# Kernel optimization log

Hardware: AMD Instinct MI355X
Metric: run time of the kernel (lower is better)

The kernel has to match this reference:

```python
import jax, jax.numpy as jnp
import numpy as np
from jax.scipy.special import gammaln

BLOCK = 96          # NIQE block size at scale 1 (48 at scale 2)
KSIZE = 7           # gaussian MSCN window size
SIGMA = 7.0 / 6.0   # gaussian sigma
PAD = KSIZE // 2
NUM_FEAT = 18       # features per block per scale

# gamma grid for AGGD shape-parameter search (matches torch.arange(0.2, 10.001, 0.001))
AGGD_GRID = jnp.asarray(np.arange(0.2, 10.0 + 0.001, 0.001), dtype=jnp.float32)
R_GAM = jnp.exp(2.0 * gammaln(2.0 / AGGD_GRID) - (gammaln(1.0 / AGGD_GRID) + gammaln(3.0 / AGGD_GRID)))


def _gauss_kernel():
    m = (KSIZE - 1) / 2.0
    y, x = np.ogrid[-m:m + 1, -m:m + 1]
    h = np.exp(-(x * x + y * y) / (2.0 * SIGMA * SIGMA))
    h[h < np.finfo(h.dtype).eps * h.max()] = 0
    h = h / h.sum()
    return jnp.asarray(h, dtype=jnp.float32)[None, None]  # (1,1,7,7)

GAUSS = _gauss_kernel()


def imfilter(x):
    # replicate ('same') padding + valid conv, like _image_filter
    xp = jnp.pad(x, ((0, 0), (0, 0), (PAD, PAD), (PAD, PAD)), mode='edge')
    return jax.lax.conv_general_dilated(xp, GAUSS, (1, 1), 'VALID')


def estimate_aggd(blocks):
    # blocks: (N, k, k)
    mask_l = blocks < 0
    mask_r = blocks > 0
    cl = jnp.sum(mask_l, axis=(-1, -2)).astype(blocks.dtype)
    cr = jnp.sum(mask_r, axis=(-1, -2)).astype(blocks.dtype)
    left_std = jnp.sqrt(jnp.sum(jnp.where(mask_l, blocks, 0.0) ** 2, axis=(-1, -2)) / (cl + 1e-8))
    right_std = jnp.sqrt(jnp.sum(jnp.where(mask_r, blocks, 0.0) ** 2, axis=(-1, -2)) / (cr + 1e-8))
    gamma_hat = left_std / right_std
    rhat = jnp.mean(jnp.abs(blocks), axis=(-1, -2)) ** 2 / jnp.mean(blocks ** 2, axis=(-1, -2))
    rhat_norm = rhat * (gamma_hat ** 3 + 1.0) * (gamma_hat + 1.0) / (gamma_hat ** 2 + 1.0) ** 2
    pos = jnp.argmin(jnp.abs(R_GAM[None, :] - rhat_norm[:, None]), axis=-1)  # (N, 9801) search
    alpha = AGGD_GRID[pos]
    conv = jnp.sqrt(jnp.exp(gammaln(1.0 / alpha) - gammaln(3.0 / alpha)))
    return alpha, left_std * conv, right_std * conv


def mscn_features(blocks):
    # blocks: (N, k, k) -> (N, 18)
    alpha, lb, rb = estimate_aggd(blocks)
    feats = [alpha, (lb + rb) / 2.0]
    for sh in ((0, 1), (1, 0), (1, 1), (1, -1)):
        shifted = jnp.roll(blocks, sh, axis=(-2, -1))
        a, l, r = estimate_aggd(blocks * shifted)
        mean = (r - l) * jnp.exp(gammaln(2.0 / a) - gammaln(1.0 / a))
        feats.extend((a, mean, l, r))
    return jnp.stack(feats, axis=-1)


def blockify(img, bs):
    # img: (b,1,H,W) -> (b, nb, bs, bs); partial blocks discarded like _blockproc_torch
    b, _, h, w = img.shape
    nbh, nbw = h // bs, w // bs
    x = img[:, 0, :nbh * bs, :nbw * bs].reshape(b, nbh, bs, nbw, bs)
    return x.transpose(0, 1, 3, 2, 4).reshape(b, nbh * nbw, bs, bs)


def mscn_normalize(img):
    mu = imfilter(img)
    sigma = jnp.sqrt(jnp.abs(imfilter(img * img) - mu * mu))
    return (img - mu) / (sigma + 1.0)


def niqe_score(image, mu_pris, cov_pris):
    img = image
    feats = []
    for scale in (1, 2):
        norm = mscn_normalize(img)
        blocks = blockify(norm, BLOCK // scale)
        b, nb, k, _ = blocks.shape
        f = mscn_features(blocks.reshape(b * nb, k, k)).reshape(b, nb, NUM_FEAT)
        feats.append(f)
        if scale == 1:
            # 2x2 average-pool downsample for second scale
            bb, cc, hh, ww = img.shape
            img = img.reshape(bb, cc, hh // 2, 2, ww // 2, 2).mean(axis=(3, 5))
    feats = jnp.concatenate(feats, axis=-1)  # (b, nb, 36)
    nb = feats.shape[1]
    mu_dist = feats.mean(axis=1)                        # (b, 36)
    xm = feats - mu_dist[:, None, :]
    cov_dist = jnp.einsum('bnf,bng->bfg', xm, xm) / (nb - 1)
    cov = (cov_pris[None] + cov_dist) / 2.0
    diff = mu_pris[None, :] - mu_dist                   # (b, 36)
    invc = jnp.linalg.pinv(cov)
    quad = jnp.einsum('bf,bfg,bg->b', diff, invc, diff)
    return jnp.sqrt(jnp.maximum(quad, 0.0))


def setup_inputs() -> dict:
    key = jax.random.key(0)
    k1, k2, k3 = jax.random.split(key, 3)
    image = jax.random.uniform(k1, (16, 1, 1056, 1056), dtype=jnp.float32)
    mu_pris = jax.random.normal(k2, (36,), dtype=jnp.float32)
    a = jax.random.normal(k3, (36, 36), dtype=jnp.float32)
    cov_pris = a @ a.T / 36.0 + 0.5 * jnp.eye(36, dtype=jnp.float32)  # SPD pristine covariance
    return {'image': image, 'mu_pris': mu_pris, 'cov_pris': cov_pris}


def reference(image, mu_pris, cov_pris):
    return niqe_score(image, mu_pris, cov_pris)
```

## Files before the change

### kernel.cpp

```cpp
#include <hip/hip_runtime.h>
#include <math.h>

#define NGRID 9801
#define NB 11
#define NBLK (NB*NB)
#define BATCH 16
#define NFEAT 36

typedef float v2f __attribute__((ext_vector_type(2)));

__global__ void init_tables(float* __restrict__ rgam, float* __restrict__ convt,
                            float* __restrict__ meanf, float* __restrict__ w1d) {
    int i = blockIdx.x * blockDim.x + threadIdx.x;
    if (i < NGRID) {
        double a = (double)(float)(0.2 + 0.001 * (double)i);
        double g1 = lgamma(1.0 / a);
        double g2 = lgamma(2.0 / a);
        double g3 = lgamma(3.0 / a);
        rgam[i]  = (float)exp(2.0 * g2 - g1 - g3);
        convt[i] = (float)sqrt(exp(g1 - g3));
        meanf[i] = (float)exp(g2 - g1);
    }
    if (i == 0) {
        double g[7], s = 0.0;
        for (int k = 0; k < 7; ++k) { double d = (double)(k - 3); g[k] = exp(-d * d * 18.0 / 49.0); s += g[k]; }
        for (int k = 0; k < 7; ++k) w1d[k] = (float)(g[k] / s);
    }
}

__device__ __forceinline__ float bperm(int addr, float v) {
    return __int_as_float(__builtin_amdgcn_ds_bpermute(addr, __float_as_int(v)));
}
__device__ __forceinline__ float dpp_getL(float v) {
    return __int_as_float(__builtin_amdgcn_update_dpp(
        0, __float_as_int(v), 0x138 , 0xF, 0xF, true));
}
__device__ __forceinline__ float dpp_getR(float v) {
    return __int_as_float(__builtin_amdgcn_update_dpp(
        0, __float_as_int(v), 0x130 , 0xF, 0xF, true));
}

template <int K, bool WDS>
__global__ __launch_bounds__(256) void fused_mscn_stats(
        const float* __restrict__ img, float* __restrict__ dsout,
        const float* __restrict__ w1d, float* __restrict__ stats) {
    constexpr int NSLAB = K / 48;
    constexpr int NSTRIP = 4 / NSLAB;
    constexpr int SROWS = K / NSTRIP;
    constexpr int W = K * NB;
    constexpr int H = W;

    __shared__ float lastrow[NSTRIP][K];
    __shared__ float edgeL[NSTRIP][NSLAB][SROWS];
    __shared__ float edgeR[NSTRIP][NSLAB][SROWS];
    __shared__ float redf[4][15];
    __shared__ float redc[4][10];

    const int tid = threadIdx.x;
    const int lane = tid & 63;
    const int wv = tid >> 6;
    const int slab = wv % NSLAB;
    const int strip = wv / NSLAB;
    const int bIdx = blockIdx.x;
    const int b = blockIdx.y;
    const int bh = bIdx / NB, bw = bIdx % NB;
    const int x0 = bw * K + slab * 48;
    const int gx = x0 - 3 + lane;
    const int gxc = min(max(gx, 0), W - 1);
    const int r0 = bh * K + strip * SROWS;
    const bool act = (lane >= 3) && (lane <= 50);
    int am1 = 0, ap1 = 0;
    if constexpr (NSLAB == 1) {
        am1 = ((lane == 3) ? 50 : (lane - 1)) << 2;
        ap1 = ((lane == 50) ? 3 : (lane + 1)) << 2;
    }

    const char* baseB = (const char*)(img + (size_t)b * H * W);
    const float w0=w1d[0], w1=w1d[1], w2=w1d[2], w3=w1d[3], w4=w1d[4], w5=w1d[5], w6=w1d[6];

    int addrB = (min(max(r0 - 3, 0), H - 1) * W + gxc) * 4;
    int rowNext = r0 - 2;
    auto ld = [&]() -> float {
        float v = *(const float*)(baseB + addrB);
        addrB += (rowNext >= 1 && rowNext < H) ? (W * 4) : 0;
        ++rowNext;
        return v;
    };

    float pa0, pa1, pa2, pa4, pa5, pa6, vHp;
    auto issue_raw = [&](float v) {
        pa2 = dpp_getL(v);
        pa1 = dpp_getL(pa2);
        pa0 = dpp_getL(pa1);
        pa4 = dpp_getR(v);
        pa5 = dpp_getR(pa4);
        pa6 = dpp_getR(pa5);
        vHp = v;
    };
    auto sq2 = [](float v) -> v2f { v2f t; t.x = v; t.y = v * v; return t; };
    auto combine_raw = [&]() -> v2f {
        v2f r = sq2(pa0) * w0;
        r += sq2(pa1) * w1;
        r += sq2(pa2) * w2;
        r += sq2(vHp) * w3;
        r += sq2(pa4) * w4;
        r += sq2(pa5) * w5;
        r += sq2(pa6) * w6;
        return r;
    };

    v2f accp[5];
    float sab[5];
    #pragma unroll
    for (int s = 0; s < 5; ++s) { accp[s] = (v2f)0.f; sab[s] = 0.f; }
    int cl[5] = {0,0,0,0,0}, cr[5] = {0,0,0,0,0};

    auto upd = [&](int s, float v) {
        float vp = fmaxf(v, 0.f);
        v2f t; t.x = vp; t.y = v;
        accp[s] += t * t;
        sab[s] += fabsf(v);
        cl[s] += __popcll(__ballot(v < 0.f));
        cr[s] += __popcll(__ballot(v > 0.f));
    };

    v2f mq0,mq1,mq2,mq3,mq4,mq5,mq6;
    float rA, rB, rC, rD;
    float vN = ld();
    { float v=vN; vN=ld(); issue_raw(v); mq0=combine_raw(); }
    { float v=vN; vN=ld(); issue_raw(v); mq1=combine_raw(); }
    { float v=vN; vN=ld(); issue_raw(v); mq2=combine_raw(); }
    { float v=vN; vN=ld(); issue_raw(v); mq3=combine_raw(); rA=v; }
    { float v=vN; vN=ld(); issue_raw(v); mq4=combine_raw(); rB=v; }
    { float v=vN; vN=ld(); issue_raw(v); mq5=combine_raw(); rC=v; }
    { float v=vN; vN=ld(); issue_raw(v); mq6=combine_raw(); rD=v; }
    { float v=vN; vN=ld(); issue_raw(v); }
    float vN2 = ld();
    float vN3 = ld();
    float vN4 = ld();

    float normP = 0.f, normP2 = 0.f;
    float pendSL = 0.f, pendPL = 0.f, pendPR = 0.f;
    float firstN = 0.f, dsSave = 0.f;
    const bool dsw = WDS && (lane & 1) && (lane >= 3) && (lane <= 49);

    #pragma unroll 4
    for (int yy = 0; yy < SROWS; ++yy) {
        const int y = r0 + yy;
        if (yy > 0) {
            upd(0, normP);
            upd(1, normP * pendSL);
            upd(2, normP * normP2);
            upd(3, normP * pendPL);
            upd(4, normP * pendPR);
        }
        v2f ms = mq0 * w0;
        ms += mq1 * w1;
        ms += mq2 * w2;
        ms += mq3 * w3;
        ms += mq4 * w4;
        ms += mq5 * w5;
        ms += mq6 * w6;
        float mu = ms.x, s2 = ms.y;
        float sig = __builtin_amdgcn_sqrtf(fabsf(s2 - mu * mu));
        float nrm = (rA - mu) * __builtin_amdgcn_rcpf(sig + 1.0f);
        float cur = act ? nrm : 0.f;

        if (yy == 0) firstN = cur;
        if constexpr (NSLAB == 2) {
            if (lane == 3)  edgeL[strip][slab][yy] = cur;
            if (lane == 50) edgeR[strip][slab][yy] = cur;
        }
        if (yy == SROWS - 1 && act) lastrow[strip][slab * 48 + lane - 3] = cur;

        if constexpr (WDS) {
            float hs = rA + dpp_getR(rA);
            if ((y & 1) == 0) dsSave = hs;
            else if (dsw)
                dsout[((size_t)b * (H / 2) + (y >> 1)) * (W / 2) + (gx >> 1)] = 0.25f * (dsSave + hs);
        }

        if constexpr (NSLAB == 2) {
            pendSL = dpp_getL(cur);
            pendPL = dpp_getL(normP);
            pendPR = dpp_getR(normP);
        } else {
            pendSL = bperm(am1, cur);
            pendPL = bperm(am1, normP);
            pendPR = bperm(ap1, normP);
        }
        normP2 = normP; normP = cur;

        v2f mh = combine_raw();
        mq0=mq1; mq1=mq2; mq2=mq3; mq3=mq4; mq4=mq5; mq5=mq6; mq6=mh;

        rA=rB; rB=rC; rC=rD; rD=vHp;
        float vv = vN; vN=vN2; vN2=vN3; vN3=vN4; vN4=ld();
        issue_raw(vv);
    }
    upd(0, normP);
    upd(1, normP * pendSL);
    upd(2, normP * normP2);
    upd(3, normP * pendPL);
    upd(4, normP * pendPR);

    __syncthreads();

    {
        const int ps = (strip + NSTRIP - 1) % NSTRIP;
        int j  = slab * 48 + (lane - 3);
        int js = act ? j : 0;
        int jm1 = (js + K - 1) % K;
        int jp1 = (js + 1) % K;
        float pv  = act ? lastrow[ps][js]  : 0.f;
        float pvL = act ? lastrow[ps][jm1] : 0.f;
        float pvR = act ? lastrow[ps][jp1] : 0.f;
        upd(2, firstN * pv);
        upd(3, firstN * pvL);
        upd(4, firstN * pvR);
    }

    if constexpr (NSLAB == 2) {
        if (lane < SROWS) {
            int r = lane;
            if (slab == 0) {
                float c0  = edgeL[strip][0][r];
                float e95 = edgeR[strip][1][r];
                upd(1, c0 * e95);
                if (r > 0) {
                    upd(3, c0 * edgeR[strip][1][r - 1]);
                    upd(4, edgeR[strip][0][r] * edgeL[strip][1][r - 1]);
                }
            } else {
                float c48 = edgeL[strip][1][r];
                float e47 = edgeR[strip][0][r];
                upd(1, c48 * e47);
                if (r > 0) {
                    upd(3, c48 * edgeR[strip][0][r - 1]);
                    upd(4, edgeR[strip][1][r] * edgeL[strip][0][r - 1]);
                }
            }
        }
    }

    #pragma unroll
    for (int off = 32; off >= 1; off >>= 1)
        #pragma unroll
        for (int s = 0; s < 5; ++s) {
            accp[s].x += __shfl_down(accp[s].x, off);
            accp[s].y += __shfl_down(accp[s].y, off);
            sab[s]    += __shfl_down(sab[s],    off);
        }
    if (lane == 0) {
        #pragma unroll
        for (int s = 0; s < 5; ++s) {
            redf[wv][s*3+0] = accp[s].x;
            redf[wv][s*3+1] = accp[s].y;
            redf[wv][s*3+2] = sab[s];
            redc[wv][s*2+0] = (float)cl[s];
            redc[wv][s*2+1] = (float)cr[s];
        }
    }
    __syncthreads();
    if (tid < 15) {
        stats[((size_t)b * NBLK + bIdx) * 25 + tid] =
            redf[0][tid] + redf[1][tid] + redf[2][tid] + redf[3][tid];
    } else if (tid < 25) {
        int t = tid - 15;
        stats[((size_t)b * NBLK + bIdx) * 25 + tid] =
            redc[0][t] + redc[1][t] + redc[2][t] + redc[3][t];
    }
}

__global__ __launch_bounds__(256) void aggd_kernel(
        const float* __restrict__ stats1, const float* __restrict__ stats2,
        const float* __restrict__ rgam, const float* __restrict__ convt,
        const float* __restrict__ meanf, float* __restrict__ feats) {
    __shared__ float rg[NGRID];
    for (int i = threadIdx.x; i < NGRID; i += 256) rg[i] = rgam[i];
    __syncthreads();

    int gid = blockIdx.x * 256 + threadIdx.x;
    if (gid >= 2 * BATCH * NBLK * 5) return;
    int s = gid % 5; int t = gid / 5;
    int blk = t % NBLK; t /= NBLK;
    int b = t % BATCH; int scale = t / BATCH;

    const float* st = (scale ? stats2 : stats1) + ((size_t)b * NBLK + blk) * 25;
    float sr2 = st[s*3+0], ssq = st[s*3+1], sab = st[s*3+2];
    float cl = st[15 + 2*s], cr = st[15 + 2*s + 1];
    float sl2 = fmaxf(ssq - sr2, 0.f);
    float n = scale ? (48.f * 48.f) : (96.f * 96.f);

    float lstd = sqrtf(sl2 / (cl + 1e-8f));
    float rstd = sqrtf(sr2 / (cr + 1e-8f));
    float gh = lstd / rstd;
    float mab = sab / n;
    float msq = ssq / n;
    float rhat = mab * mab / msq;
    float g2 = gh * gh;
    float x = rhat * (gh * g2 + 1.f) * (gh + 1.f) / ((g2 + 1.f) * (g2 + 1.f));

    int lo = 0, hi = NGRID;
    while (lo < hi) {
        int mid = (lo + hi) >> 1;
        if (rg[mid] < x) lo = mid + 1; else hi = mid;
    }
    int gi;
    if (lo <= 0) gi = 0;
    else if (lo >= NGRID) gi = NGRID - 1;
    else {
        float dlo = x - rg[lo - 1];
        float dhi = rg[lo] - x;
        gi = (dlo <= dhi) ? lo - 1 : lo;
    }

    float alpha = (float)(0.2 + 0.001 * (double)gi);
    float cv = convt[gi];
    float lb = lstd * cv, rb = rstd * cv;
    float* fo = feats + ((size_t)b * NBLK + blk) * NFEAT + (scale ? 18 : 0);
    if (s == 0) {
        fo[0] = alpha;
        fo[1] = 0.5f * (lb + rb);
    } else {
        int o = 2 + (s - 1) * 4;
        fo[o]     = alpha;
        fo[o + 1] = (rb - lb) * meanf[gi];
        fo[o + 2] = lb;
        fo[o + 3] = rb;
    }
}

__global__ __launch_bounds__(256) void score_kernel(
        const float* __restrict__ feats, const float* __restrict__ mu_pris,
        const float* __restrict__ cov_pris, float* __restrict__ out) {
    __shared__ float F[NBLK][NFEAT];
    __shared__ double mu[NFEAT];
    __shared__ double A[NFEAT][NFEAT + 1];
    __shared__ double dff[NFEAT];
    __shared__ double xs[NFEAT];
    int b = blockIdx.x, tid = threadIdx.x;
    const float* fp = feats + (size_t)b * NBLK * NFEAT;
    for (int i = tid; i < NBLK * NFEAT; i += 256) F[i / NFEAT][i % NFEAT] = fp[i];
    __syncthreads();
    if (tid < NFEAT) {
        double s = 0.0;
        for (int n = 0; n < NBLK; ++n) s += (double)F[n][tid];
        mu[tid] = s / (double)NBLK;
        dff[tid] = (double)mu_pris[tid] - mu[tid];
    }
    __syncthreads();
    for (int e = tid; e < NFEAT * NFEAT; e += 256) {
        int f = e / NFEAT, g = e % NFEAT;
        double mf = mu[f], mg = mu[g];
        double s = 0.0;
        for (int n = 0; n < NBLK; ++n) s += ((double)F[n][f] - mf) * ((double)F[n][g] - mg);
        A[f][g] = (s / (double)(NBLK - 1) + (double)cov_pris[f * NFEAT + g]) * 0.5;
    }
    if (tid < NFEAT) A[tid][NFEAT] = dff[tid];
    for (int k = 0; k < NFEAT - 1; ++k) {
        __syncthreads();
        double rk = 1.0 / A[k][k];
        for (int e = tid; e < NFEAT * (NFEAT + 1); e += 256) {
            int r = e / (NFEAT + 1), c = e % (NFEAT + 1);
            if (r > k && c > k) A[r][c] -= (A[r][k] * rk) * A[k][c];
        }
    }
    __syncthreads();
    for (int i = NFEAT - 1; i >= 0; --i) {
        if (tid == i) xs[i] = A[i][NFEAT] / A[i][i];
        __syncthreads();
        if (tid < i) A[tid][NFEAT] -= A[tid][i] * xs[i];
    }
    __syncthreads();
    if (tid == 0) {
        double quad = 0.0;
        for (int i = 0; i < NFEAT; ++i) quad += dff[i] * xs[i];
        out[b] = (float)sqrt(fmax(quad, 0.0));
    }
}

extern "C" void kernel_launch(void* const* d_in, const int* in_sizes, int n_in,
                              void* d_out, int out_size, void* d_ws, size_t ws_size,
                              hipStream_t stream) {
    const float* img      = (const float*)d_in[0];
    const float* mu_pris  = (const float*)d_in[1];
    const float* cov_pris = (const float*)d_in[2];
    float* out = (float*)d_out;
    float* ws = (float*)d_ws;

    float* rgam  = ws;
    float* convt = rgam + 9856;
    float* meanf = convt + 9856;
    float* w1d   = meanf + 9856;
    float* stats1 = w1d + 8;
    float* stats2 = stats1 + BATCH * NBLK * 25;
    float* feats  = stats2 + BATCH * NBLK * 25;
    float* dsimg  = feats + BATCH * NBLK * NFEAT;

    init_tables<<<(NGRID + 255) / 256, 256, 0, stream>>>(rgam, convt, meanf, w1d);

    fused_mscn_stats<96, true><<<dim3(NBLK, BATCH), 256, 0, stream>>>(
        img, dsimg, w1d, stats1);
    fused_mscn_stats<48, false><<<dim3(NBLK, BATCH), 256, 0, stream>>>(
        dsimg, nullptr, w1d, stats2);

    aggd_kernel<<<(2 * BATCH * NBLK * 5 + 255) / 256, 256, 0, stream>>>(
        stats1, stats2, rgam, convt, meanf, feats);

    score_kernel<<<BATCH, 256, 0, stream>>>(feats, mu_pris, cov_pris, out);
}
```

Measured before the change: 157.8 us.

## Fuse AGGD fit into score kernel, single-wave elimination, halve scale-2 block waves

Merges the AGGD parameter search and the covariance/Mahalanobis score into one per-batch kernel. Features now go to shared memory instead of a global buffer, which removes a launch and a round trip through global memory. The Gaussian elimination now runs inside a single wavefront with wave barriers instead of 35+36 block-wide __syncthreads steps. The second-scale stats kernel now launches with 2 waves (128 threads) instead of 4. In exchange, the AGGD search runs on only 16 blocks, and each re-loads the 9801-entry table into LDS, so that stage has less parallelism.

Measured after the change: 227.6 us. 1.44x slower.

```diff
diff --git a/kernel.cpp b/kernel.cpp
--- a/kernel.cpp
+++ b/kernel.cpp
@@ -40,12 +40,13 @@
         0, __float_as_int(v), 0x130 , 0xF, 0xF, true));
 }
 
-template <int K, bool WDS>
-__global__ __launch_bounds__(256) void fused_mscn_stats(
+template <int K, bool WDS, int NSTRIPT>
+__global__ __launch_bounds__((K / 48) * NSTRIPT * 64) void fused_mscn_stats(
         const float* __restrict__ img, float* __restrict__ dsout,
         const float* __restrict__ w1d, float* __restrict__ stats) {
     constexpr int NSLAB = K / 48;
-    constexpr int NSTRIP = 4 / NSLAB;
+    constexpr int NSTRIP = NSTRIPT;
+    constexpr int WAVES = NSLAB * NSTRIP;
     constexpr int SROWS = K / NSTRIP;
     constexpr int W = K * NB;
     constexpr int H = W;
@@ -53,8 +54,8 @@
     __shared__ float lastrow[NSTRIP][K];
     __shared__ float edgeL[NSTRIP][NSLAB][SROWS];
     __shared__ float edgeR[NSTRIP][NSLAB][SROWS];
-    __shared__ float redf[4][15];
-    __shared__ float redc[4][10];
+    __shared__ float redf[WAVES][15];
+    __shared__ float redc[WAVES][10];
 
     const int tid = threadIdx.x;
     const int lane = tid & 63;
@@ -263,86 +264,84 @@
     }
     __syncthreads();
     if (tid < 15) {
-        stats[((size_t)b * NBLK + bIdx) * 25 + tid] =
-            redf[0][tid] + redf[1][tid] + redf[2][tid] + redf[3][tid];
+        float s = 0.f;
+        #pragma unroll
+        for (int w = 0; w < WAVES; ++w) s += redf[w][tid];
+        stats[((size_t)b * NBLK + bIdx) * 25 + tid] = s;
     } else if (tid < 25) {
         int t = tid - 15;
-        stats[((size_t)b * NBLK + bIdx) * 25 + tid] =
-            redc[0][t] + redc[1][t] + redc[2][t] + redc[3][t];
-    }
-}
-
-__global__ __launch_bounds__(256) void aggd_kernel(
+        float s = 0.f;
+        #pragma unroll
+        for (int w = 0; w < WAVES; ++w) s += redc[w][t];
+        stats[((size_t)b * NBLK + bIdx) * 25 + tid] = s;
+    }
+}
+
+__global__ __launch_bounds__(256) void finish_kernel(
         const float* __restrict__ stats1, const float* __restrict__ stats2,
         const float* __restrict__ rgam, const float* __restrict__ convt,
-        const float* __restrict__ meanf, float* __restrict__ feats) {
+        const float* __restrict__ meanf,
+        const float* __restrict__ mu_pris, const float* __restrict__ cov_pris,
+        float* __restrict__ out) {
     __shared__ float rg[NGRID];
-    for (int i = threadIdx.x; i < NGRID; i += 256) rg[i] = rgam[i];
-    __syncthreads();
-
-    int gid = blockIdx.x * 256 + threadIdx.x;
-    if (gid >= 2 * BATCH * NBLK * 5) return;
-    int s = gid % 5; int t = gid / 5;
-    int blk = t % NBLK; t /= NBLK;
-    int b = t % BATCH; int scale = t / BATCH;
-
-    const float* st = (scale ? stats2 : stats1) + ((size_t)b * NBLK + blk) * 25;
-    float sr2 = st[s*3+0], ssq = st[s*3+1], sab = st[s*3+2];
-    float cl = st[15 + 2*s], cr = st[15 + 2*s + 1];
-    float sl2 = fmaxf(ssq - sr2, 0.f);
-    float n = scale ? (48.f * 48.f) : (96.f * 96.f);
-
-    float lstd = sqrtf(sl2 / (cl + 1e-8f));
-    float rstd = sqrtf(sr2 / (cr + 1e-8f));
-    float gh = lstd / rstd;
-    float mab = sab / n;
-    float msq = ssq / n;
-    float rhat = mab * mab / msq;
-    float g2 = gh * gh;
-    float x = rhat * (gh * g2 + 1.f) * (gh + 1.f) / ((g2 + 1.f) * (g2 + 1.f));
-
-    int lo = 0, hi = NGRID;
-    while (lo < hi) {
-        int mid = (lo + hi) >> 1;
-        if (rg[mid] < x) lo = mid + 1; else hi = mid;
-    }
-    int gi;
-    if (lo <= 0) gi = 0;
-    else if (lo >= NGRID) gi = NGRID - 1;
-    else {
-        float dlo = x - rg[lo - 1];
-        float dhi = rg[lo] - x;
-        gi = (dlo <= dhi) ? lo - 1 : lo;
-    }
-
-    float alpha = (float)(0.2 + 0.001 * (double)gi);
-    float cv = convt[gi];
-    float lb = lstd * cv, rb = rstd * cv;
-    float* fo = feats + ((size_t)b * NBLK + blk) * NFEAT + (scale ? 18 : 0);
-    if (s == 0) {
-        fo[0] = alpha;
-        fo[1] = 0.5f * (lb + rb);
-    } else {
-        int o = 2 + (s - 1) * 4;
-        fo[o]     = alpha;
-        fo[o + 1] = (rb - lb) * meanf[gi];
-        fo[o + 2] = lb;
-        fo[o + 3] = rb;
-    }
-}
-
-__global__ __launch_bounds__(256) void score_kernel(
-        const float* __restrict__ feats, const float* __restrict__ mu_pris,
-        const float* __restrict__ cov_pris, float* __restrict__ out) {
     __shared__ float F[NBLK][NFEAT];
     __shared__ double mu[NFEAT];
     __shared__ double A[NFEAT][NFEAT + 1];
     __shared__ double dff[NFEAT];
-    __shared__ double xs[NFEAT];
-    int b = blockIdx.x, tid = threadIdx.x;
-    const float* fp = feats + (size_t)b * NBLK * NFEAT;
-    for (int i = tid; i < NBLK * NFEAT; i += 256) F[i / NFEAT][i % NFEAT] = fp[i];
-    __syncthreads();
+    const int b = blockIdx.x, tid = threadIdx.x;
+
+    for (int i = tid; i < NGRID; i += 256) rg[i] = rgam[i];
+    __syncthreads();
+
+    for (int task = tid; task < 2 * NBLK * 5; task += 256) {
+        int s = task % 5; int u = task / 5;
+        int blk = u % NBLK; int scale = u / NBLK;
+        const float* st = (scale ? stats2 : stats1) + ((size_t)b * NBLK + blk) * 25;
+        float sr2 = st[s*3+0], ssq = st[s*3+1], sab = st[s*3+2];
+        float cl = st[15 + 2*s], cr = st[15 + 2*s + 1];
+        float sl2 = fmaxf(ssq - sr2, 0.f);
+        float n = scale ? (48.f * 48.f) : (96.f * 96.f);
+
+        float lstd = sqrtf(sl2 / (cl + 1e-8f));
+        float rstd = sqrtf(sr2 / (cr + 1e-8f));
+        float gh = lstd / rstd;
+        float mab = sab / n;
+        float msq = ssq / n;
+        float rhat = mab * mab / msq;
+        float g2 = gh * gh;
+        float x = rhat * (gh * g2 + 1.f) * (gh + 1.f) / ((g2 + 1.f) * (g2 + 1.f));
+
+        int lo = 0, hi = NGRID;
+        while (lo < hi) {
+            int mid = (lo + hi) >> 1;
+            if (rg[mid] < x) lo = mid + 1; else hi = mid;
+        }
+        int gi;
+        if (lo <= 0) gi = 0;
+        else if (lo >= NGRID) gi = NGRID - 1;
+        else {
+            float dlo = x - rg[lo - 1];
+            float dhi = rg[lo] - x;
+            gi = (dlo <= dhi) ? lo - 1 : lo;
+        }
+
+        float alpha = (float)(0.2 + 0.001 * (double)gi);
+        float cv = convt[gi];
+        float lb = lstd * cv, rb = rstd * cv;
+        float* fo = &F[blk][scale ? 18 : 0];
+        if (s == 0) {
+            fo[0] = alpha;
+            fo[1] = 0.5f * (lb + rb);
+        } else {
+            int o = 2 + (s - 1) * 4;
+            fo[o]     = alpha;
+            fo[o + 1] = (rb - lb) * meanf[gi];
+            fo[o + 2] = lb;
+            fo[o + 3] = rb;
+        }
+    }
+    __syncthreads();
+
     if (tid < NFEAT) {
         double s = 0.0;
         for (int n = 0; n < NBLK; ++n) s += (double)F[n][tid];
@@ -350,6 +349,7 @@
         dff[tid] = (double)mu_pris[tid] - mu[tid];
     }
     __syncthreads();
+
     for (int e = tid; e < NFEAT * NFEAT; e += 256) {
         int f = e / NFEAT, g = e % NFEAT;
         double mf = mu[f], mg = mu[g];
@@ -358,25 +358,33 @@
         A[f][g] = (s / (double)(NBLK - 1) + (double)cov_pris[f * NFEAT + g]) * 0.5;
     }
     if (tid < NFEAT) A[tid][NFEAT] = dff[tid];
-    for (int k = 0; k < NFEAT - 1; ++k) {
-        __syncthreads();
-        double rk = 1.0 / A[k][k];
-        for (int e = tid; e < NFEAT * (NFEAT + 1); e += 256) {
-            int r = e / (NFEAT + 1), c = e % (NFEAT + 1);
-            if (r > k && c > k) A[r][c] -= (A[r][k] * rk) * A[k][c];
-        }
-    }
-    __syncthreads();
-    for (int i = NFEAT - 1; i >= 0; --i) {
-        if (tid == i) xs[i] = A[i][NFEAT] / A[i][i];
-        __syncthreads();
-        if (tid < i) A[tid][NFEAT] -= A[tid][i] * xs[i];
-    }
-    __syncthreads();
-    if (tid == 0) {
-        double quad = 0.0;
-        for (int i = 0; i < NFEAT; ++i) quad += dff[i] * xs[i];
-        out[b] = (float)sqrt(fmax(quad, 0.0));
+    __syncthreads();
+
+    if (tid < 64) {
+        const int lane = tid;
+        volatile double (*Av)[NFEAT + 1] = (volatile double (*)[NFEAT + 1])A;
+        for (int k = 0; k < NFEAT - 1; ++k) {
+            double rk = 1.0 / Av[k][k];
+            double fac = 0.0;
+            if (lane > k && lane < NFEAT) fac = Av[lane][k] * rk;
+            for (int c = k + 1; c <= NFEAT; ++c) {
+                double pk = Av[k][c];
+                if (lane > k && lane < NFEAT) Av[lane][c] = Av[lane][c] - fac * pk;
+            }
+            __builtin_amdgcn_wave_barrier();
+        }
+        for (int i = NFEAT - 1; i >= 0; --i) {
+            if (lane == i) Av[i][NFEAT] = Av[i][NFEAT] / Av[i][i];
+            __builtin_amdgcn_wave_barrier();
+            double xi = Av[i][NFEAT];
+            if (lane < i) Av[lane][NFEAT] = Av[lane][NFEAT] - Av[lane][i] * xi;
+            __builtin_amdgcn_wave_barrier();
+        }
+        if (lane == 0) {
+            double quad = 0.0;
+            for (int i = 0; i < NFEAT; ++i) quad += dff[i] * Av[i][NFEAT];
+            out[b] = (float)sqrt(fmax(quad, 0.0));
+        }
     }
 }
 
@@ -395,18 +403,15 @@
     float* w1d   = meanf + 9856;
     float* stats1 = w1d + 8;
     float* stats2 = stats1 + BATCH * NBLK * 25;
-    float* feats  = stats2 + BATCH * NBLK * 25;
-    float* dsimg  = feats + BATCH * NBLK * NFEAT;
+    float* dsimg  = stats2 + BATCH * NBLK * 25;
 
     init_tables<<<(NGRID + 255) / 256, 256, 0, stream>>>(rgam, convt, meanf, w1d);
 
-    fused_mscn_stats<96, true><<<dim3(NBLK, BATCH), 256, 0, stream>>>(
+    fused_mscn_stats<96, true, 2><<<dim3(NBLK, BATCH), 256, 0, stream>>>(
         img, dsimg, w1d, stats1);
-    fused_mscn_stats<48, false><<<dim3(NBLK, BATCH), 256, 0, stream>>>(
+    fused_mscn_stats<48, false, 2><<<dim3(NBLK, BATCH), 128, 0, stream>>>(
         dsimg, nullptr, w1d, stats2);
 
-    aggd_kernel<<<(2 * BATCH * NBLK * 5 + 255) / 256, 256, 0, stream>>>(
-        stats1, stats2, rgam, convt, meanf, feats);
-
-    score_kernel<<<BATCH, 256, 0, stream>>>(feats, mu_pris, cov_pris, out);
-}
+    finish_kernel<<<BATCH, 256, 0, stream>>>(
+        stats1, stats2, rgam, convt, meanf, mu_pris, cov_pris, out);
+}
```

## Fuse both NIQE scales into one launch with on-the-fly 2x downsampling

Applied to the files above, without the earlier changes.

The two per-scale MSCN/statistics kernels become a single launch. Scale-1 and scale-2 blocks are interleaved in the grid, and the scale-2 path builds its input by averaging 2x2 pixels straight from the original image instead of reading a separately written downsampled image. This drops one kernel launch, the write and re-read of the intermediate downsampled image, and the serial dependency between the scales so both can run concurrently. In exchange, scale-2 blocks now load twice as many full-resolution rows (float2 pairs) from global memory.

Result: slower. 184.8 us (+17.1%).

```diff
diff --git a/kernel.cpp b/kernel.cpp
--- a/kernel.cpp
+++ b/kernel.cpp
@@ -40,12 +40,12 @@
         0, __float_as_int(v), 0x130 , 0xF, 0xF, true));
 }
 
-template <int K, bool WDS>
-__global__ __launch_bounds__(256) void fused_mscn_stats(
-        const float* __restrict__ img, float* __restrict__ dsout,
-        const float* __restrict__ w1d, float* __restrict__ stats) {
+template <int K, int NSTRIP, int DSF>
+__device__ __forceinline__ void fused_body(
+        const float* __restrict__ img, const float* __restrict__ w1d,
+        float* __restrict__ stats, int bIdx, int b) {
     constexpr int NSLAB = K / 48;
-    constexpr int NSTRIP = 4 / NSLAB;
+    constexpr int WAVES = NSLAB * NSTRIP;
     constexpr int SROWS = K / NSTRIP;
     constexpr int W = K * NB;
     constexpr int H = W;
@@ -53,16 +53,14 @@
     __shared__ float lastrow[NSTRIP][K];
     __shared__ float edgeL[NSTRIP][NSLAB][SROWS];
     __shared__ float edgeR[NSTRIP][NSLAB][SROWS];
-    __shared__ float redf[4][15];
-    __shared__ float redc[4][10];
+    __shared__ float redf[WAVES][15];
+    __shared__ float redc[WAVES][10];
 
     const int tid = threadIdx.x;
     const int lane = tid & 63;
     const int wv = tid >> 6;
     const int slab = wv % NSLAB;
     const int strip = wv / NSLAB;
-    const int bIdx = blockIdx.x;
-    const int b = blockIdx.y;
     const int bh = bIdx / NB, bw = bIdx % NB;
     const int x0 = bw * K + slab * 48;
     const int gx = x0 - 3 + lane;
@@ -75,14 +73,23 @@
         ap1 = ((lane == 50) ? 3 : (lane + 1)) << 2;
     }
 
-    const char* baseB = (const char*)(img + (size_t)b * H * W);
+    const char* baseB = (const char*)(img + (size_t)b * (H * DSF) * (size_t)(W * DSF));
     const float w0=w1d[0], w1=w1d[1], w2=w1d[2], w3=w1d[3], w4=w1d[4], w5=w1d[5], w6=w1d[6];
 
-    int addrB = (min(max(r0 - 3, 0), H - 1) * W + gxc) * 4;
+    int addrB;
+    if constexpr (DSF == 1) addrB = (min(max(r0 - 3, 0), H - 1) * W + gxc) * 4;
+    else addrB = (min(max(r0 - 3, 0), H - 1) * 2 * (W * 2) + 2 * gxc) * 4;
     int rowNext = r0 - 2;
     auto ld = [&]() -> float {
-        float v = *(const float*)(baseB + addrB);
-        addrB += (rowNext >= 1 && rowNext < H) ? (W * 4) : 0;
+        float v;
+        if constexpr (DSF == 1) {
+            v = *(const float*)(baseB + addrB);
+        } else {
+            float2 u = *(const float2*)(baseB + addrB);
+            float2 l = *(const float2*)(baseB + addrB + (W * DSF) * 4);
+            v = (u.x + u.y + l.x + l.y) * 0.25f;
+        }
+        addrB += (rowNext >= 1 && rowNext < H) ? (W * DSF * DSF * 4) : 0;
         ++rowNext;
         return v;
     };
@@ -141,12 +148,10 @@
 
     float normP = 0.f, normP2 = 0.f;
     float pendSL = 0.f, pendPL = 0.f, pendPR = 0.f;
-    float firstN = 0.f, dsSave = 0.f;
-    const bool dsw = WDS && (lane & 1) && (lane >= 3) && (lane <= 49);
+    float firstN = 0.f;
 
     #pragma unroll 4
     for (int yy = 0; yy < SROWS; ++yy) {
-        const int y = r0 + yy;
         if (yy > 0) {
             upd(0, normP);
             upd(1, normP * pendSL);
@@ -172,13 +177,6 @@
             if (lane == 50) edgeR[strip][slab][yy] = cur;
         }
         if (yy == SROWS - 1 && act) lastrow[strip][slab * 48 + lane - 3] = cur;
-
-        if constexpr (WDS) {
-            float hs = rA + dpp_getR(rA);
-            if ((y & 1) == 0) dsSave = hs;
-            else if (dsw)
-                dsout[((size_t)b * (H / 2) + (y >> 1)) * (W / 2) + (gx >> 1)] = 0.25f * (dsSave + hs);
-        }
 
         if constexpr (NSLAB == 2) {
             pendSL = dpp_getL(cur);
@@ -263,13 +261,26 @@
     }
     __syncthreads();
     if (tid < 15) {
-        stats[((size_t)b * NBLK + bIdx) * 25 + tid] =
-            redf[0][tid] + redf[1][tid] + redf[2][tid] + redf[3][tid];
+        float s = 0.f;
+        #pragma unroll
+        for (int w = 0; w < WAVES; ++w) s += redf[w][tid];
+        stats[((size_t)b * NBLK + bIdx) * 25 + tid] = s;
     } else if (tid < 25) {
         int t = tid - 15;
-        stats[((size_t)b * NBLK + bIdx) * 25 + tid] =
-            redc[0][t] + redc[1][t] + redc[2][t] + redc[3][t];
-    }
+        float s = 0.f;
+        #pragma unroll
+        for (int w = 0; w < WAVES; ++w) s += redc[w][t];
+        stats[((size_t)b * NBLK + bIdx) * 25 + tid] = s;
+    }
+}
+
+__global__ __launch_bounds__(256) void fused_both(
+        const float* __restrict__ img, const float* __restrict__ w1d,
+        float* __restrict__ stats1, float* __restrict__ stats2) {
+    const int scale = blockIdx.x & 1;
+    const int bIdx = blockIdx.x >> 1;
+    if (scale == 0) fused_body<96, 2, 1>(img, w1d, stats1, bIdx, blockIdx.y);
+    else            fused_body<48, 4, 2>(img, w1d, stats2, bIdx, blockIdx.y);
 }
 
 __global__ __launch_bounds__(256) void aggd_kernel(
@@ -396,14 +407,10 @@
     float* stats1 = w1d + 8;
     float* stats2 = stats1 + BATCH * NBLK * 25;
     float* feats  = stats2 + BATCH * NBLK * 25;
-    float* dsimg  = feats + BATCH * NBLK * NFEAT;
 
     init_tables<<<(NGRID + 255) / 256, 256, 0, stream>>>(rgam, convt, meanf, w1d);
 
-    fused_mscn_stats<96, true><<<dim3(NBLK, BATCH), 256, 0, stream>>>(
-        img, dsimg, w1d, stats1);
-    fused_mscn_stats<48, false><<<dim3(NBLK, BATCH), 256, 0, stream>>>(
-        dsimg, nullptr, w1d, stats2);
+    fused_both<<<dim3(2 * NBLK, BATCH), 256, 0, stream>>>(img, w1d, stats1, stats2);
 
     aggd_kernel<<<(2 * BATCH * NBLK * 5 + 255) / 256, 256, 0, stream>>>(
         stats1, stats2, rgam, convt, meanf, feats);
```

## Solve score system in fp32 registers with wavefront shuffles instead of shared-memory fp64

Applied to the files above, without the earlier changes.

Rewrites the final score kernel's Gaussian elimination so that each of 36 lanes in one 64-wide wavefront holds a matrix row in registers. Pivot rows are broadcast with shuffles, which removes the per-pivot __syncthreads barriers and the shared-memory fp64 updates. The covariance accumulation and the solve also move from double to float. This cuts barrier and fp64 latency in a small serial tail kernel, at the cost of lower numerical precision and no pivoting in fp32.

Measured after the change: 165.7 us. +5.0%, slower.

```diff
diff --git a/kernel.cpp b/kernel.cpp
--- a/kernel.cpp
+++ b/kernel.cpp
@@ -335,10 +335,9 @@
         const float* __restrict__ feats, const float* __restrict__ mu_pris,
         const float* __restrict__ cov_pris, float* __restrict__ out) {
     __shared__ float F[NBLK][NFEAT];
+    __shared__ float Af[NFEAT][NFEAT + 1];
     __shared__ double mu[NFEAT];
-    __shared__ double A[NFEAT][NFEAT + 1];
-    __shared__ double dff[NFEAT];
-    __shared__ double xs[NFEAT];
+    __shared__ float dffF[NFEAT];
     int b = blockIdx.x, tid = threadIdx.x;
     const float* fp = feats + (size_t)b * NBLK * NFEAT;
     for (int i = tid; i < NBLK * NFEAT; i += 256) F[i / NFEAT][i % NFEAT] = fp[i];
@@ -346,37 +345,53 @@
     if (tid < NFEAT) {
         double s = 0.0;
         for (int n = 0; n < NBLK; ++n) s += (double)F[n][tid];
-        mu[tid] = s / (double)NBLK;
-        dff[tid] = (double)mu_pris[tid] - mu[tid];
+        double m = s / (double)NBLK;
+        mu[tid] = m;
+        dffF[tid] = (float)((double)mu_pris[tid] - m);
     }
     __syncthreads();
     for (int e = tid; e < NFEAT * NFEAT; e += 256) {
         int f = e / NFEAT, g = e % NFEAT;
-        double mf = mu[f], mg = mu[g];
-        double s = 0.0;
-        for (int n = 0; n < NBLK; ++n) s += ((double)F[n][f] - mf) * ((double)F[n][g] - mg);
-        A[f][g] = (s / (double)(NBLK - 1) + (double)cov_pris[f * NFEAT + g]) * 0.5;
-    }
-    if (tid < NFEAT) A[tid][NFEAT] = dff[tid];
-    for (int k = 0; k < NFEAT - 1; ++k) {
-        __syncthreads();
-        double rk = 1.0 / A[k][k];
-        for (int e = tid; e < NFEAT * (NFEAT + 1); e += 256) {
-            int r = e / (NFEAT + 1), c = e % (NFEAT + 1);
-            if (r > k && c > k) A[r][c] -= (A[r][k] * rk) * A[k][c];
-        }
-    }
-    __syncthreads();
-    for (int i = NFEAT - 1; i >= 0; --i) {
-        if (tid == i) xs[i] = A[i][NFEAT] / A[i][i];
-        __syncthreads();
-        if (tid < i) A[tid][NFEAT] -= A[tid][i] * xs[i];
-    }
-    __syncthreads();
-    if (tid == 0) {
-        double quad = 0.0;
-        for (int i = 0; i < NFEAT; ++i) quad += dff[i] * xs[i];
-        out[b] = (float)sqrt(fmax(quad, 0.0));
+        float mf = (float)mu[f], mg = (float)mu[g];
+        float s = 0.f;
+        for (int n = 0; n < NBLK; ++n) s += (F[n][f] - mf) * (F[n][g] - mg);
+        Af[f][g] = (s / (float)(NBLK - 1) + cov_pris[f * NFEAT + g]) * 0.5f;
+    }
+    if (tid < NFEAT) Af[tid][NFEAT] = dffF[tid];
+    __syncthreads();
+
+    if (tid < 64) {
+        const int r = tid;
+        const int rr = (r < NFEAT) ? r : 0;
+        float a[NFEAT + 1];
+        #pragma unroll
+        for (int c = 0; c <= NFEAT; ++c) a[c] = Af[rr][c];
+
+        for (int k = 0; k < NFEAT - 1; ++k) {
+            float ark = 0.f;
+            #pragma unroll
+            for (int c = 0; c < NFEAT; ++c) if (c == k) ark = a[c];
+            float pkk = __shfl(ark, k);
+            float fac = ark / pkk;
+            #pragma unroll
+            for (int c = 0; c <= NFEAT; ++c) {
+                float pkc = __shfl(a[c], k);
+                if (c > k && r > k && r < NFEAT) a[c] -= fac * pkc;
+            }
+        }
+        float xr = 0.f;
+        for (int i = NFEAT - 1; i >= 0; --i) {
+            float ai = 0.f;
+            #pragma unroll
+            for (int c = 0; c < NFEAT; ++c) if (c == i) ai = a[c];
+            float xi = __shfl(a[NFEAT], i) / __shfl(ai, i);
+            if (r == i) xr = xi;
+            if (r < i) a[NFEAT] -= ai * xi;
+        }
+        float contrib = (r < NFEAT) ? dffF[r] * xr : 0.f;
+        #pragma unroll
+        for (int off = 32; off >= 1; off >>= 1) contrib += __shfl_down(contrib, off);
+        if (r == 0) out[b] = sqrtf(fmaxf(contrib, 0.f));
     }
 }
 
```
